# Performance work log

Measured on AMD Instinct MI355X. Metric: run time of the kernel, lower is better.

## Reference

```python
import jax, jax.numpy as jnp
import numpy as np

EXP_BITS = 5
SIG_BITS = 10


def fp_quantize_ste(x, exp_bits=EXP_BITS, sig_bits=SIG_BITS):
    """Simulate a low-precision float format (round-to-nearest, subnormals on),
    with a straight-through estimator for gradients."""
    ebias = 2 ** (exp_bits - 1) - 1
    emin = 1 - ebias                      # min normal exponent; below -> subnormal
    emax = ebias
    xmax = (2.0 - 2.0 ** (-sig_bits)) * (2.0 ** emax)

    ax = jnp.abs(x)
    # exponent of each value; guard log2(0)
    e = jnp.floor(jnp.log2(jnp.where(ax > 0, ax, 1.0)))
    # clamping e below emin quantizes subnormals on the fixed 2^(emin-sig_bits) grid;
    # clamping above emax is handled by the final saturation to +-xmax
    e = jnp.clip(e, emin, emax)
    scale = jnp.exp2(sig_bits - e)        # quantization step = 2^(e - sig_bits)
    q = jnp.round(x * scale) / scale      # round-to-nearest (rmode=1)
    q = jnp.clip(q, -xmax, xmax)
    q = jnp.where(ax > 0, q, x)           # preserve exact zeros (and signed zero)
    # straight-through estimator: forward = q, backward = identity
    return x + jax.lax.stop_gradient(q - x)


def setup_inputs() -> dict:
    key = jax.random.key(0)
    k1, k2, k3 = jax.random.split(key, 3)
    N, D_IN, D_OUT = 8192, 4096, 4096
    x = jax.random.normal(k1, (N, D_IN), dtype=jnp.float32)
    weight = jax.random.normal(k2, (D_OUT, D_IN), dtype=jnp.float32) * (D_IN ** -0.5)
    bias = jax.random.normal(k3, (D_OUT,), dtype=jnp.float32) * 0.01
    return {"x": x, "weight": weight, "bias": bias}


def reference(x, weight, bias):
    xq = fp_quantize_ste(x)               # act_quant
    wq = fp_quantize_ste(weight)          # weight_quant
    bq = fp_quantize_ste(bias)            # bias quantized with weight_quant
    # F.linear: x @ W^T + b
    return jnp.einsum('ni,oi->no', xq, wq) + bq
```

## Files before the change

### kernel.cpp

```cpp
#include <hip/hip_runtime.h>
#include <hip/hip_fp16.h>
#include <cstdint>
#include <cstddef>

#define GLOBAL_AS __attribute__((address_space(1)))
#define LDS_AS    __attribute__((address_space(3)))

typedef __attribute__((ext_vector_type(8))) _Float16 f16x8;
typedef __attribute__((ext_vector_type(4))) float    f32x4;

__device__ __forceinline__ void gload_lds16(const void* g, void* l) {
    __builtin_amdgcn_global_load_lds((const GLOBAL_AS void*)g,
                                     (LDS_AS void*)l, 16, 0, 0);
}

__device__ __forceinline__ __half qcvt(float x) {
    x = fminf(fmaxf(x, -65504.f), 65504.f);
    return __float2half(x);
}

__global__ void quant_f32_to_f16(const float* __restrict__ in,
                                 __half* __restrict__ out, int n4) {
    const int stride = gridDim.x * blockDim.x;
    for (int i = blockIdx.x * blockDim.x + threadIdx.x; i < n4; i += stride) {
        const float4 f = reinterpret_cast<const float4*>(in)[i];
        union { __half h[4]; uint2 u; } p;
        p.h[0] = qcvt(f.x);
        p.h[1] = qcvt(f.y);
        p.h[2] = qcvt(f.z);
        p.h[3] = qcvt(f.w);
        reinterpret_cast<uint2*>(out)[i] = p.u;
    }
}

__global__ __launch_bounds__(512, 2) void gemm_f16_8phase(
    const __half* __restrict__ A, const __half* __restrict__ B,
    const __half* __restrict__ bias, float* __restrict__ C,
    int M, int N, int K)
{
    __shared__ __align__(16) __half lds[2][2][2][8192];

    const int tid  = threadIdx.x;
    const int lane = tid & 63;
    const int wid  = tid >> 6;
    const int wr   = wid >> 2;
    const int wc   = wid & 3;
    const int fr   = lane & 15;
    const int fq   = lane >> 4;

    const int nwg = gridDim.x;
    const int qq = nwg >> 3, rr = nwg & 7;
    const int xcd = blockIdx.x & 7, idx = blockIdx.x >> 3;
    const int wgid = (xcd < rr ? xcd * (qq + 1)
                               : rr * (qq + 1) + (xcd - rr) * qq) + idx;
    const int nbn = N >> 8;
    const int tile_m = (wgid / nbn) << 8;
    const int tile_n = (wgid % nbn) << 8;

    const int wbyte = (lane * 16) ^ (((lane >> 5) & 1) << 5);
    const int srow  = ((wid >> 1) << 4) + (wbyte >> 6);
    const int scb   = ((wid & 1) << 6) + (wbyte & 63);
    const char* gA0 = (const char*)A + (size_t)(tile_m + srow) * K * 2 + scb;
    const char* gB0 = (const char*)B + (size_t)(tile_n + srow) * K * 2 + scb;
    const size_t rstep = (size_t)64  * K * 2;
    const size_t hstep = (size_t)128 * K * 2;
    const int ldst = tid * 16;

    const int woff  = (fr * 64 + fq * 16) ^ (((fr >> 3) & 1) << 5);
    const int aoff  = wr * 8192 + woff;
    const int boff  = wc * 4096 + woff;

    f32x4 acc[2][2][4][2];
#pragma unroll
    for (int qa = 0; qa < 2; ++qa)
#pragma unroll
        for (int qb = 0; qb < 2; ++qb)
#pragma unroll
            for (int m = 0; m < 4; ++m)
#pragma unroll
                for (int n = 0; n < 2; ++n)
                    acc[qa][qb][m][n] = (f32x4){0.f, 0.f, 0.f, 0.f};

    f16x8 af[4][2], bf[2][2];

#define STAGE_A(bufi, h, kt) do {                                          \
        char* l_ = (char*)(&lds[bufi][0][h][0]) + ldst;                    \
        const char* g_ = gA0 + (size_t)(kt) * 128 + ((h) ? hstep : 0);     \
        gload_lds16(g_, l_);                                               \
        gload_lds16(g_ + rstep, l_ + 8192);                                \
    } while (0)

#define STAGE_B(bufi, h, kt) do {                                          \
        char* l_ = (char*)(&lds[bufi][1][h][0]) + ldst;                    \
        const char* g_ = gB0 + (size_t)(kt) * 128 + ((h) ? hstep : 0);     \
        gload_lds16(g_, l_);                                               \
        gload_lds16(g_ + rstep, l_ + 8192);                                \
    } while (0)

#define LDA(bufi, qa) do {                                                 \
        const char* lb_ = (const char*)(&lds[bufi][0][qa][0]) + aoff;      \
        _Pragma("unroll")                                                  \
        for (int m_ = 0; m_ < 4; ++m_) {                                   \
            af[m_][0] = *(const f16x8*)(lb_ + m_ * 2048);                  \
            af[m_][1] = *(const f16x8*)(lb_ + m_ * 2048 + 1024);           \
        }                                                                  \
    } while (0)

#define LDB(bufi, hb) do {                                                 \
        const char* lb_ = (const char*)(&lds[bufi][1][hb][0]) + boff;      \
        _Pragma("unroll")                                                  \
        for (int n_ = 0; n_ < 2; ++n_) {                                   \
            bf[n_][0] = *(const f16x8*)(lb_ + n_ * 2048);                  \
            bf[n_][1] = *(const f16x8*)(lb_ + n_ * 2048 + 1024);           \
        }                                                                  \
    } while (0)

#define MMA(qa, qb)                                                        \
    __builtin_amdgcn_s_setprio(1);                                         \
    _Pragma("unroll")                                                      \
    for (int m_ = 0; m_ < 4; ++m_) {                                       \
        _Pragma("unroll")                                                  \
        for (int n_ = 0; n_ < 2; ++n_) {                                   \
            acc[qa][qb][m_][n_] = __builtin_amdgcn_mfma_f32_16x16x32_f16(  \
                af[m_][0], bf[n_][0], acc[qa][qb][m_][n_], 0, 0, 0);       \
            acc[qa][qb][m_][n_] = __builtin_amdgcn_mfma_f32_16x16x32_f16(  \
                af[m_][1], bf[n_][1], acc[qa][qb][m_][n_], 0, 0, 0);       \
        }                                                                  \
    }                                                                      \
    __builtin_amdgcn_s_setprio(0);

#define PH_BAR1()                                                          \
    asm volatile("" ::: "memory");                                         \
    __builtin_amdgcn_s_barrier();                                          \
    asm volatile("s_waitcnt lgkmcnt(0)" ::: "memory")

#define PH_BAR2()                                                          \
    asm volatile("" ::: "memory");                                         \
    __builtin_amdgcn_s_barrier()

#define TILE_FULL(cur, nxt, kt)                                            \
    LDA(cur, 0); LDB(cur, 0); STAGE_B(nxt, 0, (kt) + 1);                   \
    PH_BAR1(); MMA(0, 0); PH_BAR2();                                       \
    LDB(cur, 1); STAGE_A(cur, 0, (kt) + 2);                                \
    PH_BAR1(); MMA(0, 1); PH_BAR2();                                       \
    LDA(cur, 1); STAGE_B(cur, 1, (kt) + 2);                                \
    PH_BAR1(); MMA(1, 1); PH_BAR2();                                       \
    LDB(cur, 0); STAGE_A(cur, 1, (kt) + 2);                                \
    asm volatile("s_waitcnt vmcnt(6)" ::: "memory");                       \
    PH_BAR1(); MMA(1, 0); PH_BAR2();

    STAGE_A(0, 0, 0); STAGE_B(0, 0, 0); STAGE_B(0, 1, 0); STAGE_A(0, 1, 0);
    STAGE_A(1, 0, 1); STAGE_B(1, 1, 1); STAGE_A(1, 1, 1);
    asm volatile("s_waitcnt vmcnt(6)" ::: "memory");
    __builtin_amdgcn_s_barrier();

    const int nt = K >> 6;
    for (int kt = 0; kt + 3 < nt; kt += 2) {
        TILE_FULL(0, 1, kt);
        TILE_FULL(1, 0, kt + 1);
    }

    LDA(0, 0); LDB(0, 0); STAGE_B(1, 0, nt - 1);
    PH_BAR1(); MMA(0, 0); PH_BAR2();
    LDB(0, 1);
    PH_BAR1(); MMA(0, 1); PH_BAR2();
    LDA(0, 1);
    PH_BAR1(); MMA(1, 1); PH_BAR2();
    LDB(0, 0);
    asm volatile("s_waitcnt vmcnt(0)" ::: "memory");
    PH_BAR1(); MMA(1, 0); PH_BAR2();

    LDA(1, 0); LDB(1, 0);
    PH_BAR1(); MMA(0, 0); PH_BAR2();
    LDB(1, 1);
    PH_BAR1(); MMA(0, 1); PH_BAR2();
    LDA(1, 1);
    PH_BAR1(); MMA(1, 1); PH_BAR2();
    LDB(1, 0);
    PH_BAR1(); MMA(1, 0);

    float bv[2][2];
#pragma unroll
    for (int qb = 0; qb < 2; ++qb)
#pragma unroll
        for (int n = 0; n < 2; ++n)
            bv[qb][n] = __half2float(
                bias[tile_n + qb * 128 + wc * 32 + n * 16 + fr]);

#pragma unroll
    for (int qa = 0; qa < 2; ++qa)
#pragma unroll
        for (int qb = 0; qb < 2; ++qb)
#pragma unroll
            for (int m = 0; m < 4; ++m)
#pragma unroll
                for (int n = 0; n < 2; ++n) {
                    const int col = tile_n + qb * 128 + wc * 32 + n * 16 + fr;
                    const int rowb = tile_m + qa * 128 + wr * 64 + m * 16 + fq * 4;
#pragma unroll
                    for (int r = 0; r < 4; ++r)
                        C[(size_t)(rowb + r) * N + col] =
                            acc[qa][qb][m][n][r] + bv[qb][n];
                }

#undef STAGE_A
#undef STAGE_B
#undef LDA
#undef LDB
#undef MMA
#undef PH_BAR1
#undef PH_BAR2
#undef TILE_FULL
}

__global__ void qat_gemm_naive(const float* __restrict__ A,
                               const float* __restrict__ B,
                               const float* __restrict__ bias,
                               float* __restrict__ C, int M, int N, int K) {
    const int col = blockIdx.x * blockDim.x + threadIdx.x;
    const int row = blockIdx.y;
    if (col >= N || row >= M) return;
    float s = 0.f;
    for (int k = 0; k < K; ++k) {
        float a = __half2float(qcvt(A[(size_t)row * K + k]));
        float b = __half2float(qcvt(B[(size_t)col * K + k]));
        s += a * b;
    }
    C[(size_t)row * N + col] = s + __half2float(qcvt(bias[col]));
}

extern "C" void kernel_launch(void* const* d_in, const int* in_sizes, int n_in,
                              void* d_out, int out_size, void* d_ws,
                              size_t ws_size, hipStream_t stream) {
    const float* x = (const float*)d_in[0];
    const float* w = (const float*)d_in[1];
    const float* b = (const float*)d_in[2];
    float* out = (float*)d_out;

    const int xn = in_sizes[0];
    const int wn = in_sizes[1];
    const int N  = in_sizes[2];
    const int K  = wn / N;
    const int M  = xn / K;

    const size_t need = (size_t)(xn + wn + N) * sizeof(__half);
    const bool ok = (M % 256 == 0) && (N % 256 == 0) &&
                    (K % 128 == 0) && (K >= 256);

    if (ws_size >= need && ok) {
        __half* xq = (__half*)d_ws;
        __half* wq = xq + xn;
        __half* bq = wq + wn;

        int blk;
        blk = (xn / 4 + 255) / 256; if (blk > 2048) blk = 2048;
        quant_f32_to_f16<<<blk, 256, 0, stream>>>(x, xq, xn / 4);
        blk = (wn / 4 + 255) / 256; if (blk > 2048) blk = 2048;
        quant_f32_to_f16<<<blk, 256, 0, stream>>>(w, wq, wn / 4);
        blk = (N / 4 + 255) / 256; if (blk > 2048) blk = 2048;
        quant_f32_to_f16<<<blk, 256, 0, stream>>>(b, bq, N / 4);

        dim3 grid((M / 256) * (N / 256));
        gemm_f16_8phase<<<grid, 512, 0, stream>>>(xq, wq, bq, out, M, N, K);
    } else {
        dim3 grid((N + 255) / 256, M);
        qat_gemm_naive<<<grid, 256, 0, stream>>>(x, w, b, out, M, N, K);
    }
}
```

Measured before the change: 296.2 us.

## Register double-buffer LDS fragments and prefetch next tile during last MMA phase

Splits the A and B register fragments into separate buffers (afX/afY, alternating b0e/b0o) so A and B fragments are reused across phases instead of reloaded from LDS. The next k-tile's first fragments are read while the final MMA phase of the current tile runs, with sched_group_barrier interleaving the LDS reads and MFMAs. It also drops the explicit lgkmcnt(0) wait after each barrier and leaves ordering to the compiler. This cuts LDS read traffic and hides LDS latency, at the cost of more VGPRs, which may lower occupancy or cause spills.

Result: slower. 820.3 us (+177.0%).

```diff
diff --git a/kernel.cpp b/kernel.cpp
--- a/kernel.cpp
+++ b/kernel.cpp
@@ -81,7 +81,9 @@
                 for (int n = 0; n < 2; ++n)
                     acc[qa][qb][m][n] = (f32x4){0.f, 0.f, 0.f, 0.f};
 
-    f16x8 af[4][2], bf[2][2];
+    f16x8 afX[4][2], afY[4][2];
+    f16x8 bfB[2][2];
+    f16x8 b0e[2][2], b0o[2][2];
 
 #define STAGE_A(bufi, h, kt) do {                                          \
         char* l_ = (char*)(&lds[bufi][0][h][0]) + ldst;                    \
@@ -97,87 +99,91 @@
         gload_lds16(g_ + rstep, l_ + 8192);                                \
     } while (0)
 
-#define LDA(bufi, qa) do {                                                 \
+#define LDGA(dst, bufi, qa) do {                                           \
         const char* lb_ = (const char*)(&lds[bufi][0][qa][0]) + aoff;      \
         _Pragma("unroll")                                                  \
         for (int m_ = 0; m_ < 4; ++m_) {                                   \
-            af[m_][0] = *(const f16x8*)(lb_ + m_ * 2048);                  \
-            af[m_][1] = *(const f16x8*)(lb_ + m_ * 2048 + 1024);           \
+            dst[m_][0] = *(const f16x8*)(lb_ + m_ * 2048);                 \
+            dst[m_][1] = *(const f16x8*)(lb_ + m_ * 2048 + 1024);          \
         }                                                                  \
     } while (0)
 
-#define LDB(bufi, hb) do {                                                 \
+#define LDGB(dst, bufi, hb) do {                                           \
         const char* lb_ = (const char*)(&lds[bufi][1][hb][0]) + boff;      \
         _Pragma("unroll")                                                  \
         for (int n_ = 0; n_ < 2; ++n_) {                                   \
-            bf[n_][0] = *(const f16x8*)(lb_ + n_ * 2048);                  \
-            bf[n_][1] = *(const f16x8*)(lb_ + n_ * 2048 + 1024);           \
+            dst[n_][0] = *(const f16x8*)(lb_ + n_ * 2048);                 \
+            dst[n_][1] = *(const f16x8*)(lb_ + n_ * 2048 + 1024);          \
         }                                                                  \
     } while (0)
 
-#define MMA(qa, qb)                                                        \
+#define MMA(qa, qb, AF, BF)                                                \
     __builtin_amdgcn_s_setprio(1);                                         \
     _Pragma("unroll")                                                      \
     for (int m_ = 0; m_ < 4; ++m_) {                                       \
         _Pragma("unroll")                                                  \
         for (int n_ = 0; n_ < 2; ++n_) {                                   \
             acc[qa][qb][m_][n_] = __builtin_amdgcn_mfma_f32_16x16x32_f16(  \
-                af[m_][0], bf[n_][0], acc[qa][qb][m_][n_], 0, 0, 0);       \
+                AF[m_][0], BF[n_][0], acc[qa][qb][m_][n_], 0, 0, 0);       \
             acc[qa][qb][m_][n_] = __builtin_amdgcn_mfma_f32_16x16x32_f16(  \
-                af[m_][1], bf[n_][1], acc[qa][qb][m_][n_], 0, 0, 0);       \
+                AF[m_][1], BF[n_][1], acc[qa][qb][m_][n_], 0, 0, 0);       \
         }                                                                  \
     }                                                                      \
     __builtin_amdgcn_s_setprio(0);
 
-#define PH_BAR1()                                                          \
+#define PH_BAR()                                                           \
     asm volatile("" ::: "memory");                                         \
     __builtin_amdgcn_s_barrier();                                          \
-    asm volatile("s_waitcnt lgkmcnt(0)" ::: "memory")
-
-#define PH_BAR2()                                                          \
-    asm volatile("" ::: "memory");                                         \
-    __builtin_amdgcn_s_barrier()
-
-#define TILE_FULL(cur, nxt, kt)                                            \
-    LDA(cur, 0); LDB(cur, 0); STAGE_B(nxt, 0, (kt) + 1);                   \
-    PH_BAR1(); MMA(0, 0); PH_BAR2();                                       \
-    LDB(cur, 1); STAGE_A(cur, 0, (kt) + 2);                                \
-    PH_BAR1(); MMA(0, 1); PH_BAR2();                                       \
-    LDA(cur, 1); STAGE_B(cur, 1, (kt) + 2);                                \
-    PH_BAR1(); MMA(1, 1); PH_BAR2();                                       \
-    LDB(cur, 0); STAGE_A(cur, 1, (kt) + 2);                                \
+    asm volatile("" ::: "memory")
+
+#define SGB_READS_THEN_MMA()                                               \
+    __builtin_amdgcn_sched_group_barrier(0x100, 12, 0);                    \
+    __builtin_amdgcn_sched_group_barrier(0x008, 16, 0)
+
+#define TILE_FULL(cur, nxt, kt, B0C, B0N)                                  \
+    LDGB(bfB, cur, 1); STAGE_B(nxt, 0, (kt) + 1);                          \
+    PH_BAR(); MMA(0, 0, afX, B0C); PH_BAR();                               \
+    LDGA(afY, cur, 1); STAGE_A(cur, 0, (kt) + 2);                          \
+    PH_BAR(); MMA(0, 1, afX, bfB); PH_BAR();                               \
+    STAGE_B(cur, 1, (kt) + 2);                                             \
+    PH_BAR(); MMA(1, 1, afY, bfB); PH_BAR();                               \
+    STAGE_A(cur, 1, (kt) + 2);                                             \
     asm volatile("s_waitcnt vmcnt(6)" ::: "memory");                       \
-    PH_BAR1(); MMA(1, 0); PH_BAR2();
+    PH_BAR();                                                              \
+    LDGA(afX, nxt, 0); LDGB(B0N, nxt, 0);                                  \
+    SGB_READS_THEN_MMA();                                                  \
+    MMA(1, 0, afY, B0C); PH_BAR();
 
     STAGE_A(0, 0, 0); STAGE_B(0, 0, 0); STAGE_B(0, 1, 0); STAGE_A(0, 1, 0);
     STAGE_A(1, 0, 1); STAGE_B(1, 1, 1); STAGE_A(1, 1, 1);
     asm volatile("s_waitcnt vmcnt(6)" ::: "memory");
     __builtin_amdgcn_s_barrier();
+    asm volatile("" ::: "memory");
+    LDGA(afX, 0, 0); LDGB(b0e, 0, 0);
 
     const int nt = K >> 6;
     for (int kt = 0; kt + 3 < nt; kt += 2) {
-        TILE_FULL(0, 1, kt);
-        TILE_FULL(1, 0, kt + 1);
-    }
-
-    LDA(0, 0); LDB(0, 0); STAGE_B(1, 0, nt - 1);
-    PH_BAR1(); MMA(0, 0); PH_BAR2();
-    LDB(0, 1);
-    PH_BAR1(); MMA(0, 1); PH_BAR2();
-    LDA(0, 1);
-    PH_BAR1(); MMA(1, 1); PH_BAR2();
-    LDB(0, 0);
+        TILE_FULL(0, 1, kt,     b0e, b0o);
+        TILE_FULL(1, 0, kt + 1, b0o, b0e);
+    }
+
+    LDGB(bfB, 0, 1); STAGE_B(1, 0, nt - 1);
+    PH_BAR(); MMA(0, 0, afX, b0e); PH_BAR();
+    LDGA(afY, 0, 1);
+    PH_BAR(); MMA(0, 1, afX, bfB); PH_BAR();
+    PH_BAR(); MMA(1, 1, afY, bfB); PH_BAR();
     asm volatile("s_waitcnt vmcnt(0)" ::: "memory");
-    PH_BAR1(); MMA(1, 0); PH_BAR2();
-
-    LDA(1, 0); LDB(1, 0);
-    PH_BAR1(); MMA(0, 0); PH_BAR2();
-    LDB(1, 1);
-    PH_BAR1(); MMA(0, 1); PH_BAR2();
-    LDA(1, 1);
-    PH_BAR1(); MMA(1, 1); PH_BAR2();
-    LDB(1, 0);
-    PH_BAR1(); MMA(1, 0);
+    PH_BAR();
+    LDGA(afX, 1, 0); LDGB(b0o, 1, 0);
+    SGB_READS_THEN_MMA();
+    MMA(1, 0, afY, b0e); PH_BAR();
+
+    LDGB(bfB, 1, 1);
+    PH_BAR(); MMA(0, 0, afX, b0o); PH_BAR();
+    LDGA(afY, 1, 1);
+    PH_BAR(); MMA(0, 1, afX, bfB); PH_BAR();
+    PH_BAR(); MMA(1, 1, afY, bfB); PH_BAR();
+    PH_BAR(); MMA(1, 0, afY, b0o);
 
     float bv[2][2];
 #pragma unroll
@@ -205,11 +211,11 @@
 
 #undef STAGE_A
 #undef STAGE_B
-#undef LDA
-#undef LDB
+#undef LDGA
+#undef LDGB
 #undef MMA
-#undef PH_BAR1
-#undef PH_BAR2
+#undef PH_BAR
+#undef SGB_READS_THEN_MMA
 #undef TILE_FULL
 }
 
```
